# Optimization experiments

Measured on AMD Instinct MI355X. Metric: run time of the kernel, lower is better.

## Reference

```python
import jax, jax.numpy as jnp
import numpy as np

B, T, D, K = 64, 1024, 256, 1024
DECAY = 0.99      # ema_decay
BETA = 0.25       # commitment_cost
EPS = 1e-5


def setup_inputs() -> dict:
    key = jax.random.key(0)
    k1, k2 = jax.random.split(key, 2)
    z = jax.random.normal(k1, (B, T, D), dtype=jnp.float32)
    # nn.init.uniform_(embedding.weight, -1/K, 1/K)
    embed = jax.random.uniform(k2, (K, D), dtype=jnp.float32,
                               minval=-1.0 / K, maxval=1.0 / K)
    ema_count = jnp.zeros((K,), dtype=jnp.float32)
    ema_weight = embed  # buffer initialized as a clone of the weight
    return {"z": z, "embed": embed, "ema_count": ema_count, "ema_weight": ema_weight}


def reference(z, embed, ema_count, ema_weight):
    Bq, Tq, Dq = z.shape
    zf = z.reshape(-1, Dq)  # [N, D], N = B*T
    # squared euclidean distances: [N, K]
    dist = (zf * zf).sum(axis=1, keepdims=True) \
        - 2.0 * (zf @ embed.T) \
        + (embed * embed).sum(axis=1)
    idx = jnp.argmin(dist, axis=1)                      # [N]
    q = embed[idx].reshape(Bq, Tq, Dq)                  # nearest codebook vectors

    commit = jnp.mean((z - jax.lax.stop_gradient(q)) ** 2)
    codebook = jnp.mean((q - jax.lax.stop_gradient(z)) ** 2)
    vq_loss = codebook + BETA * commit

    # straight-through estimator
    q_st = z + jax.lax.stop_gradient(q - z)

    # EMA codebook update (training-mode, no_grad in torch)
    counts = jax.ops.segment_sum(jnp.ones((zf.shape[0],), zf.dtype), idx, num_segments=K)
    dw = jax.ops.segment_sum(zf, idx, num_segments=K)   # one_hot.T @ z_flat, [K, D]
    new_count = DECAY * ema_count + (1.0 - DECAY) * counts
    new_ema_w = DECAY * ema_weight + (1.0 - DECAY) * dw
    n = new_count.sum()
    cs = (new_count + EPS) / (n + K * EPS) * n          # laplace-smoothed counts
    new_embed = new_ema_w / cs[:, None]

    return (q_st, vq_loss, idx.reshape(Bq, Tq), new_embed, new_count, new_ema_w)
```

## Files before the change

### kernel.cpp

```cpp
#include <hip/hip_runtime.h>
#include <cfloat>

#define N_Q     65536
#define D_DIM   256
#define K_CODES 1024
#define DELTA   0.004f
#define MARGIN  0.001f
#define SW_CAP  1536
#define SPILL_CAP 65536

#define OUT_QST   0
#define OUT_LOSS  16777216
#define OUT_IDX   16777217
#define OUT_EMBED 16842753
#define OUT_COUNT 17104897
#define OUT_EMAW  17105921

#define WS_IDX    0u
#define WS_ZZ     262144u
#define WS_PERM   524288u
#define WS_PACK   786432u
#define WS_EN     1310720u
#define WS_ICNT   1314816u
#define WS_OFFS   1318912u
#define WS_OFFW   1323008u
#define WS_CNTF   1327104u
#define WS_CS     1331200u
#define WS_ET     1335296u
#define WS_LOSSB  1859584u
#define WS_SPCNT  1867776u

typedef short          bf16x8 __attribute__((ext_vector_type(8)));
typedef unsigned short u16x8  __attribute__((ext_vector_type(8)));
typedef float          f32x4  __attribute__((ext_vector_type(4)));

__device__ inline unsigned short f2bf(float x) {
    unsigned u = __float_as_uint(x);
    u += 0x7FFFu + ((u >> 16) & 1u);
    return (unsigned short)(u >> 16);
}
__device__ inline float bf2f(unsigned short h) {
    return __uint_as_float((unsigned)h << 16);
}
__device__ inline u16x8 pack8(float4 a, float4 b) {
    u16x8 p;
    p[0]=f2bf(a.x); p[1]=f2bf(a.y); p[2]=f2bf(a.z); p[3]=f2bf(a.w);
    p[4]=f2bf(b.x); p[5]=f2bf(b.y); p[6]=f2bf(b.z); p[7]=f2bf(b.w);
    return p;
}
__device__ inline void gll16(const void* g, void* l) {
    __builtin_amdgcn_global_load_lds(
        (const __attribute__((address_space(1))) unsigned int*)g,
        (__attribute__((address_space(3))) unsigned int*)l, 16, 0, 0);
}
#define DPPMIN(x, CTRL) fminf((x), __int_as_float( \
    __builtin_amdgcn_update_dpp(0, __float_as_int(x), (CTRL), 0xF, 0xF, false)))

__global__ void prep_kernel(const float* __restrict__ embed,
                            unsigned short* __restrict__ et,
                            unsigned long long* __restrict__ pack,
                            float* __restrict__ enorm,
                            int* __restrict__ icnt,
                            double* __restrict__ lossb,
                            int* __restrict__ spc)
{
    int b = blockIdx.x, t = threadIdx.x;
    if (b < 128) {
        int tid = b * 256 + t;
        int k16 = tid >> 9, d8 = (tid >> 4) & 31, col = tid & 15;
        const float* src = &embed[(size_t)(k16 * 16 + col) * D_DIM + d8 * 8];
        float4 a = *(const float4*)&src[0];
        float4 c = *(const float4*)&src[4];
        *(u16x8*)&et[(size_t)tid * 8] = pack8(a, c);
        unsigned long long* p = pack + (size_t)tid * 2;
        p[0] = ~0ull; p[1] = ~0ull;
    } else {
        int b2 = b - 128;
        int wave = t >> 6, lane = t & 63;
        int rbase = (b2 * 4 + wave) * 8;
        for (int i = 0; i < 8; ++i) {
            int r = rbase + i;
            const float4 v = *(const float4*)&embed[(size_t)r * D_DIM + lane * 4];
            float s = v.x * v.x + v.y * v.y + v.z * v.z + v.w * v.w;
            #pragma unroll
            for (int m = 32; m >= 1; m >>= 1) s += __shfl_down(s, m, 64);
            if (lane == 0) enorm[r] = s;
        }
        if (b2 == 0) {
            #pragma unroll
            for (int i = 0; i < 4; ++i) {
                icnt[t * 4 + i] = 0;
                lossb[t * 4 + i] = 0.0;
            }
            if (t == 0) *spc = 0;
        }
    }
}

__launch_bounds__(512, 4)
__global__ void sweep_kernel(const float* __restrict__ z,
                             const float* __restrict__ embed,
                             const unsigned short* __restrict__ et,
                             const float* __restrict__ enorm,
                             float* __restrict__ zzg,
                             unsigned long long* __restrict__ pack,
                             unsigned* __restrict__ spill,
                             int* __restrict__ spc)
{
    __shared__ unsigned short Eb[2][16384];
    __shared__ unsigned list[SW_CAP];
    __shared__ unsigned short s1h[SW_CAP];
    __shared__ float Ens[K_CODES];
    __shared__ float rminS[128];
    __shared__ float zzS[128];
    __shared__ int lcnt;

    const int t = threadIdx.x;
    const int w = t >> 6, lane = t & 63;
    const int col = lane & 15, quad = lane >> 4;
    const int qbase = blockIdx.x * 128;

    if (t == 0) lcnt = 0;
    for (int i = t; i < K_CODES; i += 512) Ens[i] = enorm[i];

    {
        const unsigned short* src = et + w * 2048 + lane * 8;
        unsigned short* dst = &Eb[0][w * 2048];
        #pragma unroll
        for (int i = 0; i < 4; ++i) gll16(src + i * 512, dst + i * 512);
    }

    bf16x8 A[8];
    {
        float s = 0.f;
        #pragma unroll
        for (int ds = 0; ds < 8; ++ds) {
            const float* zp = &z[(size_t)(qbase + w*16 + col) * D_DIM
                                 + ds*32 + quad*8];
            float4 a = *(const float4*)zp;
            float4 b = *(const float4*)(zp + 4);
            s += a.x*a.x + a.y*a.y + a.z*a.z + a.w*a.w
               + b.x*b.x + b.y*b.y + b.z*b.z + b.w*b.w;
            u16x8 p = pack8(a, b);
            A[ds] = *(bf16x8*)&p;
        }
        s += __shfl_xor(s, 16, 64);
        s += __shfl_xor(s, 32, 64);
        if (quad == 0) {
            zzg[qbase + w*16 + col] = s;
            zzS[w*16 + col] = s;
        }
    }

    float rmin[4];
    #pragma unroll
    for (int i = 0; i < 4; ++i) rmin[i] = FLT_MAX;

    asm volatile("s_waitcnt vmcnt(0) lgkmcnt(0)" ::: "memory");
    __builtin_amdgcn_s_barrier();
    __builtin_amdgcn_sched_barrier(0);

    #pragma unroll 1
    for (int kc = 0; kc < 16; ++kc) {
        if (kc < 15) {
            const unsigned short* src = et + (kc + 1) * 16384 + w * 2048 + lane * 8;
            unsigned short* dst = &Eb[(kc + 1) & 1][w * 2048];
            #pragma unroll
            for (int i = 0; i < 4; ++i) gll16(src + i * 512, dst + i * 512);
        }

        const unsigned short* buf = Eb[kc & 1];
        f32x4 acc[4];
        #pragma unroll
        for (int ct = 0; ct < 4; ++ct)
            acc[ct] = (f32x4){0.f, 0.f, 0.f, 0.f};

        #pragma unroll
        for (int ds = 0; ds < 8; ++ds) {
            bf16x8 B[4];
            #pragma unroll
            for (int ct = 0; ct < 4; ++ct)
                B[ct] = *(const bf16x8*)&buf[((ct*32 + ds*4 + quad)*16 + col)*8];
            #pragma unroll
            for (int ct = 0; ct < 4; ++ct)
                acc[ct] = __builtin_amdgcn_mfma_f32_16x16x32_bf16(A[ds], B[ct], acc[ct], 0, 0, 0);
        }

        float en4[4];
        #pragma unroll
        for (int ct = 0; ct < 4; ++ct) en4[ct] = Ens[kc*64 + ct*16 + col];

        float s1v[4][4];
        #pragma unroll
        for (int ct = 0; ct < 4; ++ct)
            #pragma unroll
            for (int rg = 0; rg < 4; ++rg)
                s1v[ct][rg] = fmaf(-2.0f, acc[ct][rg], en4[ct]);

        float m4[4];
        #pragma unroll
        for (int rg = 0; rg < 4; ++rg)
            m4[rg] = fminf(fminf(s1v[0][rg], s1v[1][rg]),
                           fminf(s1v[2][rg], s1v[3][rg]));

        #pragma unroll
        for (int i = 0; i < 4; ++i) m4[i] = DPPMIN(m4[i], 0xB1);
        #pragma unroll
        for (int i = 0; i < 4; ++i) m4[i] = DPPMIN(m4[i], 0x4E);
        #pragma unroll
        for (int i = 0; i < 4; ++i) m4[i] = DPPMIN(m4[i], 0x124);
        #pragma unroll
        for (int i = 0; i < 4; ++i) m4[i] = DPPMIN(m4[i], 0x128);

        float thrv[4];
        #pragma unroll
        for (int i = 0; i < 4; ++i) {
            rmin[i] = fminf(rmin[i], m4[i]);
            thrv[i] = rmin[i] + DELTA;
        }

        #pragma unroll
        for (int rg = 0; rg < 4; ++rg) {
            float th = thrv[rg];
            #pragma unroll
            for (int ct = 0; ct < 4; ++ct) {
                if (s1v[ct][rg] <= th) {
                    int k    = kc*64 + ct*16 + col;
                    int qloc = w*16 + quad*4 + rg;
                    int pos  = atomicAdd(&lcnt, 1);
                    if (pos < SW_CAP) {
                        list[pos] = ((unsigned)qloc << 10) | (unsigned)k;
                        s1h[pos]  = f2bf(s1v[ct][rg]);
                    } else {
                        int sp = atomicAdd(spc, 1);
                        if (sp < SPILL_CAP) {
                            spill[sp] = ((unsigned)(qbase + qloc) << 10)
                                      | (unsigned)k;
                            asm volatile("s_waitcnt vmcnt(0)" ::: "memory");
                        }
                    }
                }
            }
        }

        asm volatile("s_waitcnt vmcnt(4)" ::: "memory");
        __builtin_amdgcn_s_barrier();
        __builtin_amdgcn_sched_barrier(0);
    }

    if (col == 0) {
        #pragma unroll
        for (int rg = 0; rg < 4; ++rg)
            rminS[w*16 + quad*4 + rg] = rmin[rg];
    }
    asm volatile("s_waitcnt lgkmcnt(0)" ::: "memory");
    __builtin_amdgcn_s_barrier();
    __builtin_amdgcn_sched_barrier(0);
    asm volatile("" ::: "memory");

    int cnt = lcnt; if (cnt > SW_CAP) cnt = SW_CAP;
    int gid = t >> 3, gl = t & 7;
    for (int e = gid; e < cnt; e += 64) {
        unsigned ent = list[e];
        int qloc = (int)(ent >> 10), k = (int)(ent & 1023u);
        if (bf2f(s1h[e]) > rminS[qloc] + (DELTA + MARGIN)) continue;
        int qg = qbase + qloc;
        const float* zp  = &z[(size_t)qg * D_DIM + gl * 32];
        const float* epf = &embed[(size_t)k * D_DIM + gl * 32];
        double d0 = 0.0, d1 = 0.0;
        #pragma unroll
        for (int i = 0; i < 4; ++i) {
            float4 a  = *(const float4*)&zp[i*8];
            float4 b  = *(const float4*)&epf[i*8];
            float4 c  = *(const float4*)&zp[i*8 + 4];
            float4 dv = *(const float4*)&epf[i*8 + 4];
            d0 += (double)a.x*b.x + (double)a.y*b.y + (double)a.z*b.z + (double)a.w*b.w;
            d1 += (double)c.x*dv.x + (double)c.y*dv.y + (double)c.z*dv.z + (double)c.w*dv.w;
        }
        double dd = d0 + d1;
        #pragma unroll
        for (int m = 1; m < 8; m <<= 1) dd += __shfl_xor(dd, m, 64);
        if (gl == 0) {
            float s = (zzS[qloc] - 2.0f*(float)dd) + Ens[k];
            unsigned long long pk =
                ((unsigned long long)__float_as_uint(s) << 32) | (unsigned)k;
            atomicMin(&pack[qg], pk);
        }
    }
}

__global__ void spill_kernel(const float* __restrict__ z,
                             const float* __restrict__ embed,
                             const float* __restrict__ enorm,
                             const float* __restrict__ zz,
                             const unsigned* __restrict__ spill,
                             const int* __restrict__ spc,
                             unsigned long long* __restrict__ pack)
{
    int cnt = *spc; if (cnt > SPILL_CAP) cnt = SPILL_CAP;
    int gid = (blockIdx.x * 256 + threadIdx.x) >> 3, gl = threadIdx.x & 7;
    int stride = (gridDim.x * 256) >> 3;
    for (int e = gid; e < cnt; e += stride) {
        unsigned ent = spill[e];
        int qg = (int)(ent >> 10), k = (int)(ent & 1023u);
        const float* zp  = &z[(size_t)qg * D_DIM + gl * 32];
        const float* epf = &embed[(size_t)k * D_DIM + gl * 32];
        double dd = 0.0;
        #pragma unroll
        for (int i = 0; i < 8; ++i) {
            float4 a = *(const float4*)&zp[i*4];
            float4 b = *(const float4*)&epf[i*4];
            dd += (double)a.x*b.x + (double)a.y*b.y
                + (double)a.z*b.z + (double)a.w*b.w;
        }
        #pragma unroll
        for (int m = 1; m < 8; m <<= 1) dd += __shfl_xor(dd, m, 64);
        if (gl == 0) {
            float s = (zz[qg] - 2.0f*(float)dd) + enorm[k];
            unsigned long long pk =
                ((unsigned long long)__float_as_uint(s) << 32) | (unsigned)k;
            atomicMin(&pack[qg], pk);
        }
    }
}

__global__ void qst_unpack_kernel(const unsigned long long* __restrict__ pack,
                                  const float* __restrict__ z,
                                  const float* __restrict__ embed,
                                  int* __restrict__ idx_i,
                                  float* __restrict__ idx_f,
                                  int* __restrict__ icnt,
                                  float* __restrict__ qst,
                                  double* __restrict__ lossb)
{
    __shared__ int ks[4];
    int b = blockIdx.x, t = threadIdx.x;
    int n0 = b * 4;
    if (t < 4) {
        int k = (int)(pack[n0 + t] & 0xffffffffull);
        ks[t] = k;
        idx_i[n0 + t] = k;
        idx_f[n0 + t] = (float)k;
        atomicAdd(&icnt[k], 1);
    }
    __syncthreads();
    int e0 = b * 1024 + t * 4;
    int qi = t >> 6;
    int d  = (t * 4) & 255;
    int k  = ks[qi];
    const float4 q4 = *(const float4*)&embed[(size_t)k * D_DIM + d];
    const float4 z4 = *(const float4*)&z[e0];
    float4 o;
    o.x = z4.x + (q4.x - z4.x);
    o.y = z4.y + (q4.y - z4.y);
    o.z = z4.z + (q4.z - z4.z);
    o.w = z4.w + (q4.w - z4.w);
    *(float4*)&qst[e0] = o;
    float dx = z4.x - q4.x, dy = z4.y - q4.y, dz = z4.z - q4.z, dw = z4.w - q4.w;
    float s = dx * dx + dy * dy + dz * dz + dw * dw;
    #pragma unroll
    for (int m = 32; m >= 1; m >>= 1) s += __shfl_down(s, m, 64);
    __shared__ float ps[4];
    int wave = t >> 6, lane = t & 63;
    if (lane == 0) ps[wave] = s;
    __syncthreads();
    if (t == 0)
        atomicAdd(&lossb[b & 1023],
                  (double)((ps[0] + ps[1]) + (ps[2] + ps[3])));
}

__global__ void scan_kernel(const int* __restrict__ icnt,
                            int* __restrict__ offs,
                            int* __restrict__ offw,
                            float* __restrict__ cntf)
{
    __shared__ int s[1024];
    int t = threadIdx.x;
    int v0 = icnt[t];
    s[t] = v0;
    __syncthreads();
    for (int d = 1; d < 1024; d <<= 1) {
        int v = (t >= d) ? s[t - d] : 0;
        __syncthreads();
        s[t] += v;
        __syncthreads();
    }
    int excl = s[t] - v0;
    offs[t] = excl;
    offw[t] = excl;
    cntf[t] = (float)v0;
}

__global__ void fill_kernel(const int* __restrict__ idx,
                            int* __restrict__ offw,
                            int* __restrict__ perm)
{
    int n = blockIdx.x * 256 + threadIdx.x;
    int k = idx[n];
    int pos = atomicAdd(&offw[k], 1);
    perm[pos] = n;
}

__global__ void fin_counts_kernel(const float* __restrict__ ema_count,
                                  const float* __restrict__ cntf,
                                  const double* __restrict__ lossb,
                                  float* __restrict__ out_count,
                                  float* __restrict__ out_loss,
                                  float* __restrict__ cs)
{
    __shared__ float  red[1024];
    __shared__ double dred[1024];
    int t = threadIdx.x;
    float c = 0.99f * ema_count[t] + 0.01f * cntf[t];
    out_count[t] = c;
    red[t]  = c;
    dred[t] = lossb[t];
    __syncthreads();
    for (int s = 512; s >= 1; s >>= 1) {
        if (t < s) { red[t] += red[t + s]; dred[t] += dred[t + s]; }
        __syncthreads();
    }
    float n = red[0];
    cs[t] = (c + 1e-5f) / (n + 1024.0f * 1e-5f) * n;
    if (t == 0) {
        float m = (float)(dred[0] / (double)((size_t)N_Q * D_DIM));
        out_loss[0] = m + 0.25f * m;
    }
}

__global__ void accum_embed_kernel(const float* __restrict__ z,
                                   const int* __restrict__ perm,
                                   const int* __restrict__ icnt,
                                   const int* __restrict__ offs,
                                   const float* __restrict__ cs,
                                   const float* __restrict__ ema_w,
                                   float* __restrict__ out_embed,
                                   float* __restrict__ out_emaw)
{
    __shared__ int rows[256];
    int k = blockIdx.x, t = threadIdx.x;
    int cnt = icnt[k], off = offs[k];
    double a0 = 0.0, a1 = 0.0, a2 = 0.0, a3 = 0.0;
    for (int base = 0; base < cnt; base += 256) {
        int m = min(256, cnt - base);
        __syncthreads();
        if (t < m) rows[t] = perm[off + base + t];
        __syncthreads();
        int r = 0;
        for (; r + 4 <= m; r += 4) {
            a0 += (double)z[(size_t)rows[r+0] * D_DIM + t];
            a1 += (double)z[(size_t)rows[r+1] * D_DIM + t];
            a2 += (double)z[(size_t)rows[r+2] * D_DIM + t];
            a3 += (double)z[(size_t)rows[r+3] * D_DIM + t];
        }
        for (; r < m; ++r) a0 += (double)z[(size_t)rows[r] * D_DIM + t];
    }
    double acc = (a0 + a1) + (a2 + a3);
    float w = 0.99f * ema_w[(size_t)k * D_DIM + t] + 0.01f * (float)acc;
    out_emaw[(size_t)k * D_DIM + t]  = w;
    out_embed[(size_t)k * D_DIM + t] = w / cs[k];
}

extern "C" void kernel_launch(void* const* d_in, const int* in_sizes, int n_in,
                              void* d_out, int out_size, void* d_ws, size_t ws_size,
                              hipStream_t stream)
{
    const float* z          = (const float*)d_in[0];
    const float* embed      = (const float*)d_in[1];
    const float* ema_count  = (const float*)d_in[2];
    const float* ema_weight = (const float*)d_in[3];
    float* out = (float*)d_out;
    char*  ws  = (char*)d_ws;

    int*      ws_idx  = (int*)(ws + WS_IDX);
    unsigned* ws_spill= (unsigned*)(ws + WS_IDX);
    float*    ws_zz   = (float*)(ws + WS_ZZ);
    int*      ws_perm = (int*)(ws + WS_PERM);
    unsigned long long* ws_pack = (unsigned long long*)(ws + WS_PACK);
    float*    ws_en   = (float*)(ws + WS_EN);
    int*      ws_icnt = (int*)(ws + WS_ICNT);
    int*      ws_offs = (int*)(ws + WS_OFFS);
    int*      ws_offw = (int*)(ws + WS_OFFW);
    float*    ws_cntf = (float*)(ws + WS_CNTF);
    float*    ws_cs   = (float*)(ws + WS_CS);
    unsigned short* ws_et = (unsigned short*)(ws + WS_ET);
    double*   ws_lb   = (double*)(ws + WS_LOSSB);
    int*      ws_spc  = (int*)(ws + WS_SPCNT);

    prep_kernel<<<160, 256, 0, stream>>>(embed, ws_et, ws_pack, ws_en,
                                         ws_icnt, ws_lb, ws_spc);

    sweep_kernel<<<N_Q / 128, 512, 0, stream>>>(z, embed, ws_et, ws_en, ws_zz,
                                                ws_pack, ws_spill, ws_spc);

    spill_kernel<<<32, 256, 0, stream>>>(z, embed, ws_en, ws_zz,
                                         ws_spill, ws_spc, ws_pack);

    qst_unpack_kernel<<<N_Q / 4, 256, 0, stream>>>(ws_pack, z, embed,
                                                   ws_idx, out + OUT_IDX,
                                                   ws_icnt, out + OUT_QST, ws_lb);
    scan_kernel<<<1, 1024, 0, stream>>>(ws_icnt, ws_offs, ws_offw, ws_cntf);
    fill_kernel<<<N_Q / 256, 256, 0, stream>>>(ws_idx, ws_offw, ws_perm);
    fin_counts_kernel<<<1, 1024, 0, stream>>>(ema_count, ws_cntf, ws_lb,
                                              out + OUT_COUNT, out + OUT_LOSS, ws_cs);
    accum_embed_kernel<<<K_CODES, 256, 0, stream>>>(z, ws_perm, ws_icnt, ws_offs,
                                                    ws_cs, ema_weight,
                                                    out + OUT_EMBED, out + OUT_EMAW);
}
```

Measured before the change: 271.4 us.

## Switch sweep to 32x32 MFMA tiles and split codebook across two block sets

The sweep kernel now uses 32x32x16 bf16 MFMA with 256 queries per block. The codebook is split into two halves of 512 codes, each handled by a separate set of blocks, so the grid stays at 512 blocks. The prep kernel re-lays out the bf16 codebook to match the new B-operand fragment order, and the candidate list capacity is doubled. This is meant to cut LDS traffic per FLOP and raise MFMA efficiency. In exchange each query's z tile is loaded and converted twice, each set finds only a partial row minimum so more candidates pass the threshold, the per-stage wait becomes a full vmcnt(0), and register pressure rises with 16 A fragments and 16 running minima.

```diff
diff --git a/kernel.cpp b/kernel.cpp
--- a/kernel.cpp
+++ b/kernel.cpp
@@ -6,7 +6,7 @@
 #define K_CODES 1024
 #define DELTA   0.004f
 #define MARGIN  0.001f
-#define SW_CAP  1536
+#define SW_CAP  3072
 #define SPILL_CAP 65536
 
 #define OUT_QST   0
@@ -32,7 +32,7 @@
 
 typedef short          bf16x8 __attribute__((ext_vector_type(8)));
 typedef unsigned short u16x8  __attribute__((ext_vector_type(8)));
-typedef float          f32x4  __attribute__((ext_vector_type(4)));
+typedef float          f32x16 __attribute__((ext_vector_type(16)));
 
 __device__ inline unsigned short f2bf(float x) {
     unsigned u = __float_as_uint(x);
@@ -67,8 +67,11 @@
     int b = blockIdx.x, t = threadIdx.x;
     if (b < 128) {
         int tid = b * 256 + t;
-        int k16 = tid >> 9, d8 = (tid >> 4) & 31, col = tid & 15;
-        const float* src = &embed[(size_t)(k16 * 16 + col) * D_DIM + d8 * 8];
+        int g = tid >> 10, rem = tid & 1023;
+        int s = rem >> 6, lane = rem & 63;
+        int row = g * 32 + (lane & 31);
+        int d0  = s * 16 + (lane >> 5) * 8;
+        const float* src = &embed[(size_t)row * D_DIM + d0];
         float4 a = *(const float4*)&src[0];
         float4 c = *(const float4*)&src[4];
         *(u16x8*)&et[(size_t)tid * 8] = pack8(a, c);
@@ -107,54 +110,55 @@
                              unsigned* __restrict__ spill,
                              int* __restrict__ spc)
 {
-    __shared__ unsigned short Eb[2][16384];
+    __shared__ unsigned short Eb[2][8192];
     __shared__ unsigned list[SW_CAP];
     __shared__ unsigned short s1h[SW_CAP];
-    __shared__ float Ens[K_CODES];
-    __shared__ float rminS[128];
-    __shared__ float zzS[128];
+    __shared__ float Ens[512];
+    __shared__ float rminS[256];
+    __shared__ float zzS[256];
     __shared__ int lcnt;
 
     const int t = threadIdx.x;
     const int w = t >> 6, lane = t & 63;
-    const int col = lane & 15, quad = lane >> 4;
-    const int qbase = blockIdx.x * 128;
+    const int c32 = lane & 31, hi = lane >> 5;
+    const int set = blockIdx.x >> 8;
+    const int qb  = blockIdx.x & 255;
+    const int qbase = qb * 256;
+    const int koff  = set * 512;
 
     if (t == 0) lcnt = 0;
-    for (int i = t; i < K_CODES; i += 512) Ens[i] = enorm[i];
+    Ens[t] = enorm[koff + t];
 
     {
-        const unsigned short* src = et + w * 2048 + lane * 8;
-        unsigned short* dst = &Eb[0][w * 2048];
-        #pragma unroll
-        for (int i = 0; i < 4; ++i) gll16(src + i * 512, dst + i * 512);
-    }
-
-    bf16x8 A[8];
+        const unsigned short* src = et + (size_t)(set*16 + 0) * 8192 + w*1024 + lane*8;
+        unsigned short* dst = &Eb[0][w * 1024];
+        gll16(src, dst);
+        gll16(src + 512, dst + 512);
+    }
+
+    bf16x8 Aq[16];
     {
-        float s = 0.f;
-        #pragma unroll
-        for (int ds = 0; ds < 8; ++ds) {
-            const float* zp = &z[(size_t)(qbase + w*16 + col) * D_DIM
-                                 + ds*32 + quad*8];
-            float4 a = *(const float4*)zp;
-            float4 b = *(const float4*)(zp + 4);
-            s += a.x*a.x + a.y*a.y + a.z*a.z + a.w*a.w
-               + b.x*b.x + b.y*b.y + b.z*b.z + b.w*b.w;
+        const float* zrow = &z[(size_t)(qbase + w*32 + c32) * D_DIM + hi*8];
+        float s2 = 0.f;
+        #pragma unroll
+        for (int s = 0; s < 16; ++s) {
+            float4 a = *(const float4*)&zrow[s*16];
+            float4 b = *(const float4*)&zrow[s*16 + 4];
+            s2 += a.x*a.x + a.y*a.y + a.z*a.z + a.w*a.w
+                + b.x*b.x + b.y*b.y + b.z*b.z + b.w*b.w;
             u16x8 p = pack8(a, b);
-            A[ds] = *(bf16x8*)&p;
-        }
-        s += __shfl_xor(s, 16, 64);
-        s += __shfl_xor(s, 32, 64);
-        if (quad == 0) {
-            zzg[qbase + w*16 + col] = s;
-            zzS[w*16 + col] = s;
-        }
-    }
-
-    float rmin[4];
+            Aq[s] = *(bf16x8*)&p;
+        }
+        float zz = s2 + __shfl_xor(s2, 32, 64);
+        if (lane < 32) {
+            zzS[w*32 + c32] = zz;
+            if (set == 0) zzg[qbase + w*32 + c32] = zz;
+        }
+    }
+
+    float rmin[16];
     #pragma unroll
-    for (int i = 0; i < 4; ++i) rmin[i] = FLT_MAX;
+    for (int r = 0; r < 16; ++r) rmin[r] = FLT_MAX;
 
     asm volatile("s_waitcnt vmcnt(0) lgkmcnt(0)" ::: "memory");
     __builtin_amdgcn_s_barrier();
@@ -163,100 +167,70 @@
     #pragma unroll 1
     for (int kc = 0; kc < 16; ++kc) {
         if (kc < 15) {
-            const unsigned short* src = et + (kc + 1) * 16384 + w * 2048 + lane * 8;
-            unsigned short* dst = &Eb[(kc + 1) & 1][w * 2048];
-            #pragma unroll
-            for (int i = 0; i < 4; ++i) gll16(src + i * 512, dst + i * 512);
+            const unsigned short* src =
+                et + (size_t)(set*16 + kc + 1) * 8192 + w*1024 + lane*8;
+            unsigned short* dst = &Eb[(kc + 1) & 1][w * 1024];
+            gll16(src, dst);
+            gll16(src + 512, dst + 512);
         }
 
         const unsigned short* buf = Eb[kc & 1];
-        f32x4 acc[4];
-        #pragma unroll
-        for (int ct = 0; ct < 4; ++ct)
-            acc[ct] = (f32x4){0.f, 0.f, 0.f, 0.f};
-
-        #pragma unroll
-        for (int ds = 0; ds < 8; ++ds) {
-            bf16x8 B[4];
-            #pragma unroll
-            for (int ct = 0; ct < 4; ++ct)
-                B[ct] = *(const bf16x8*)&buf[((ct*32 + ds*4 + quad)*16 + col)*8];
-            #pragma unroll
-            for (int ct = 0; ct < 4; ++ct)
-                acc[ct] = __builtin_amdgcn_mfma_f32_16x16x32_bf16(A[ds], B[ct], acc[ct], 0, 0, 0);
-        }
-
-        float en4[4];
-        #pragma unroll
-        for (int ct = 0; ct < 4; ++ct) en4[ct] = Ens[kc*64 + ct*16 + col];
-
-        float s1v[4][4];
-        #pragma unroll
-        for (int ct = 0; ct < 4; ++ct)
-            #pragma unroll
-            for (int rg = 0; rg < 4; ++rg)
-                s1v[ct][rg] = fmaf(-2.0f, acc[ct][rg], en4[ct]);
-
-        float m4[4];
-        #pragma unroll
-        for (int rg = 0; rg < 4; ++rg)
-            m4[rg] = fminf(fminf(s1v[0][rg], s1v[1][rg]),
-                           fminf(s1v[2][rg], s1v[3][rg]));
-
-        #pragma unroll
-        for (int i = 0; i < 4; ++i) m4[i] = DPPMIN(m4[i], 0xB1);
-        #pragma unroll
-        for (int i = 0; i < 4; ++i) m4[i] = DPPMIN(m4[i], 0x4E);
-        #pragma unroll
-        for (int i = 0; i < 4; ++i) m4[i] = DPPMIN(m4[i], 0x124);
-        #pragma unroll
-        for (int i = 0; i < 4; ++i) m4[i] = DPPMIN(m4[i], 0x128);
-
-        float thrv[4];
-        #pragma unroll
-        for (int i = 0; i < 4; ++i) {
-            rmin[i] = fminf(rmin[i], m4[i]);
-            thrv[i] = rmin[i] + DELTA;
-        }
-
-        #pragma unroll
-        for (int rg = 0; rg < 4; ++rg) {
-            float th = thrv[rg];
-            #pragma unroll
-            for (int ct = 0; ct < 4; ++ct) {
-                if (s1v[ct][rg] <= th) {
-                    int k    = kc*64 + ct*16 + col;
-                    int qloc = w*16 + quad*4 + rg;
-                    int pos  = atomicAdd(&lcnt, 1);
-                    if (pos < SW_CAP) {
-                        list[pos] = ((unsigned)qloc << 10) | (unsigned)k;
-                        s1h[pos]  = f2bf(s1v[ct][rg]);
-                    } else {
-                        int sp = atomicAdd(spc, 1);
-                        if (sp < SPILL_CAP) {
-                            spill[sp] = ((unsigned)(qbase + qloc) << 10)
-                                      | (unsigned)k;
-                            asm volatile("s_waitcnt vmcnt(0)" ::: "memory");
-                        }
+        f32x16 acc;
+        #pragma unroll
+        for (int i = 0; i < 16; ++i) acc[i] = 0.f;
+
+        #pragma unroll
+        for (int s = 0; s < 16; ++s) {
+            bf16x8 B = *(const bf16x8*)&buf[s*512 + lane*8];
+            acc = __builtin_amdgcn_mfma_f32_32x32x16_bf16(Aq[s], B, acc, 0, 0, 0);
+        }
+
+        float en = Ens[kc*32 + c32];
+        acc = en - 2.0f * acc;
+
+        #pragma unroll
+        for (int r = 0; r < 16; ++r) {
+            float mv = acc[r];
+            mv = DPPMIN(mv, 0xB1);
+            mv = DPPMIN(mv, 0x4E);
+            mv = DPPMIN(mv, 0x124);
+            mv = DPPMIN(mv, 0x128);
+            rmin[r] = fminf(rmin[r], mv);
+            float th = rmin[r] + DELTA;
+            if (acc[r] <= th) {
+                int k    = koff + kc*32 + c32;
+                int qloc = w*32 + (r & 3) + 8*(r >> 2) + 4*hi;
+                int pos  = atomicAdd(&lcnt, 1);
+                if (pos < SW_CAP) {
+                    list[pos] = ((unsigned)qloc << 10) | (unsigned)k;
+                    s1h[pos]  = f2bf(acc[r]);
+                } else {
+                    int sp = atomicAdd(spc, 1);
+                    if (sp < SPILL_CAP) {
+                        spill[sp] = ((unsigned)(qbase + qloc) << 10)
+                                  | (unsigned)k;
+                        asm volatile("s_waitcnt vmcnt(0)" ::: "memory");
                     }
                 }
             }
         }
 
-        asm volatile("s_waitcnt vmcnt(4)" ::: "memory");
+        asm volatile("s_waitcnt vmcnt(0)" ::: "memory");
         __builtin_amdgcn_s_barrier();
         __builtin_amdgcn_sched_barrier(0);
     }
 
-    if (col == 0) {
-        #pragma unroll
-        for (int rg = 0; rg < 4; ++rg)
-            rminS[w*16 + quad*4 + rg] = rmin[rg];
+    #pragma unroll
+    for (int r = 0; r < 16; ++r)
+        rmin[r] = fminf(rmin[r], __shfl_xor(rmin[r], 16, 64));
+    if (c32 == 0) {
+        #pragma unroll
+        for (int r = 0; r < 16; ++r)
+            rminS[w*32 + (r & 3) + 8*(r >> 2) + 4*hi] = rmin[r];
     }
     asm volatile("s_waitcnt lgkmcnt(0)" ::: "memory");
     __builtin_amdgcn_s_barrier();
     __builtin_amdgcn_sched_barrier(0);
-    asm volatile("" ::: "memory");
 
     int cnt = lcnt; if (cnt > SW_CAP) cnt = SW_CAP;
     int gid = t >> 3, gl = t & 7;
@@ -281,7 +255,7 @@
         #pragma unroll
         for (int m = 1; m < 8; m <<= 1) dd += __shfl_xor(dd, m, 64);
         if (gl == 0) {
-            float s = (zzS[qloc] - 2.0f*(float)dd) + Ens[k];
+            float s = (zzS[qloc] - 2.0f*(float)dd) + Ens[k & 511];
             unsigned long long pk =
                 ((unsigned long long)__float_as_uint(s) << 32) | (unsigned)k;
             atomicMin(&pack[qg], pk);
@@ -490,8 +464,8 @@
     prep_kernel<<<160, 256, 0, stream>>>(embed, ws_et, ws_pack, ws_en,
                                          ws_icnt, ws_lb, ws_spc);
 
-    sweep_kernel<<<N_Q / 128, 512, 0, stream>>>(z, embed, ws_et, ws_en, ws_zz,
-                                                ws_pack, ws_spill, ws_spc);
+    sweep_kernel<<<512, 512, 0, stream>>>(z, embed, ws_et, ws_en, ws_zz,
+                                          ws_pack, ws_spill, ws_spc);
 
     spill_kernel<<<32, 256, 0, stream>>>(z, embed, ws_en, ws_zz,
                                          ws_spill, ws_spc, ws_pack);
```

Result: slower. 378.1 us (+39.3%).

## Halve sweep codebook chunk for higher occupancy and fuse scan with count finalization

Applied to the files above, without the earlier changes.

The sweep kernel now streams the bf16 codebook in 32-code chunks instead of 64, halving the double-buffered LDS tile and the accumulator registers, and raises the launch-bounds occupancy hint from 4 to 6 blocks. This aims to fit more blocks per CU to hide latency, at the cost of twice as many loop iterations, barriers and DPP min reductions. Separately, the single-block scan and count-finalization kernels are merged into one launch, dropping a kernel launch and the intermediate float count buffer.

```diff
diff --git a/kernel.cpp b/kernel.cpp
--- a/kernel.cpp
+++ b/kernel.cpp
@@ -97,7 +97,7 @@
     }
 }
 
-__launch_bounds__(512, 4)
+__launch_bounds__(512, 6)
 __global__ void sweep_kernel(const float* __restrict__ z,
                              const float* __restrict__ embed,
                              const unsigned short* __restrict__ et,
@@ -107,7 +107,7 @@
                              unsigned* __restrict__ spill,
                              int* __restrict__ spc)
 {
-    __shared__ unsigned short Eb[2][16384];
+    __shared__ unsigned short Eb[2][8192];
     __shared__ unsigned list[SW_CAP];
     __shared__ unsigned short s1h[SW_CAP];
     __shared__ float Ens[K_CODES];
@@ -124,10 +124,10 @@
     for (int i = t; i < K_CODES; i += 512) Ens[i] = enorm[i];
 
     {
-        const unsigned short* src = et + w * 2048 + lane * 8;
-        unsigned short* dst = &Eb[0][w * 2048];
-        #pragma unroll
-        for (int i = 0; i < 4; ++i) gll16(src + i * 512, dst + i * 512);
+        const unsigned short* src = et + w * 1024 + lane * 8;
+        unsigned short* dst = &Eb[0][w * 1024];
+        gll16(src, dst);
+        gll16(src + 512, dst + 512);
     }
 
     bf16x8 A[8];
@@ -161,47 +161,43 @@
     __builtin_amdgcn_sched_barrier(0);
 
     #pragma unroll 1
-    for (int kc = 0; kc < 16; ++kc) {
-        if (kc < 15) {
-            const unsigned short* src = et + (kc + 1) * 16384 + w * 2048 + lane * 8;
-            unsigned short* dst = &Eb[(kc + 1) & 1][w * 2048];
-            #pragma unroll
-            for (int i = 0; i < 4; ++i) gll16(src + i * 512, dst + i * 512);
+    for (int kc = 0; kc < 32; ++kc) {
+        if (kc < 31) {
+            const unsigned short* src = et + (kc + 1) * 8192 + w * 1024 + lane * 8;
+            unsigned short* dst = &Eb[(kc + 1) & 1][w * 1024];
+            gll16(src, dst);
+            gll16(src + 512, dst + 512);
         }
 
         const unsigned short* buf = Eb[kc & 1];
-        f32x4 acc[4];
-        #pragma unroll
-        for (int ct = 0; ct < 4; ++ct)
+        f32x4 acc[2];
+        #pragma unroll
+        for (int ct = 0; ct < 2; ++ct)
             acc[ct] = (f32x4){0.f, 0.f, 0.f, 0.f};
 
         #pragma unroll
         for (int ds = 0; ds < 8; ++ds) {
-            bf16x8 B[4];
-            #pragma unroll
-            for (int ct = 0; ct < 4; ++ct)
-                B[ct] = *(const bf16x8*)&buf[((ct*32 + ds*4 + quad)*16 + col)*8];
-            #pragma unroll
-            for (int ct = 0; ct < 4; ++ct)
-                acc[ct] = __builtin_amdgcn_mfma_f32_16x16x32_bf16(A[ds], B[ct], acc[ct], 0, 0, 0);
-        }
-
-        float en4[4];
-        #pragma unroll
-        for (int ct = 0; ct < 4; ++ct) en4[ct] = Ens[kc*64 + ct*16 + col];
-
-        float s1v[4][4];
-        #pragma unroll
-        for (int ct = 0; ct < 4; ++ct)
+            bf16x8 B0 = *(const bf16x8*)&buf[((      ds*4 + quad)*16 + col)*8];
+            bf16x8 B1 = *(const bf16x8*)&buf[((32 + ds*4 + quad)*16 + col)*8];
+            acc[0] = __builtin_amdgcn_mfma_f32_16x16x32_bf16(A[ds], B0, acc[0], 0, 0, 0);
+            acc[1] = __builtin_amdgcn_mfma_f32_16x16x32_bf16(A[ds], B1, acc[1], 0, 0, 0);
+        }
+
+        float en2[2];
+        #pragma unroll
+        for (int ct = 0; ct < 2; ++ct) en2[ct] = Ens[kc*32 + ct*16 + col];
+
+        float s1v[2][4];
+        #pragma unroll
+        for (int ct = 0; ct < 2; ++ct)
             #pragma unroll
             for (int rg = 0; rg < 4; ++rg)
-                s1v[ct][rg] = fmaf(-2.0f, acc[ct][rg], en4[ct]);
+                s1v[ct][rg] = fmaf(-2.0f, acc[ct][rg], en2[ct]);
 
         float m4[4];
         #pragma unroll
         for (int rg = 0; rg < 4; ++rg)
-            m4[rg] = fminf(fminf(s1v[0][rg], s1v[1][rg]),
-                           fminf(s1v[2][rg], s1v[3][rg]));
+            m4[rg] = fminf(s1v[0][rg], s1v[1][rg]);
 
         #pragma unroll
         for (int i = 0; i < 4; ++i) m4[i] = DPPMIN(m4[i], 0xB1);
@@ -223,9 +219,9 @@
         for (int rg = 0; rg < 4; ++rg) {
             float th = thrv[rg];
             #pragma unroll
-            for (int ct = 0; ct < 4; ++ct) {
+            for (int ct = 0; ct < 2; ++ct) {
                 if (s1v[ct][rg] <= th) {
-                    int k    = kc*64 + ct*16 + col;
+                    int k    = kc*32 + ct*16 + col;
                     int qloc = w*16 + quad*4 + rg;
                     int pos  = atomicAdd(&lcnt, 1);
                     if (pos < SW_CAP) {
@@ -243,7 +239,7 @@
             }
         }
 
-        asm volatile("s_waitcnt vmcnt(4)" ::: "memory");
+        asm volatile("s_waitcnt vmcnt(2)" ::: "memory");
         __builtin_amdgcn_s_barrier();
         __builtin_amdgcn_sched_barrier(0);
     }
@@ -369,12 +365,18 @@
                   (double)((ps[0] + ps[1]) + (ps[2] + ps[3])));
 }
 
-__global__ void scan_kernel(const int* __restrict__ icnt,
-                            int* __restrict__ offs,
-                            int* __restrict__ offw,
-                            float* __restrict__ cntf)
+__global__ void scan_fin_kernel(const int* __restrict__ icnt,
+                                const float* __restrict__ ema_count,
+                                const double* __restrict__ lossb,
+                                int* __restrict__ offs,
+                                int* __restrict__ offw,
+                                float* __restrict__ out_count,
+                                float* __restrict__ out_loss,
+                                float* __restrict__ cs)
 {
     __shared__ int s[1024];
+    __shared__ float  red[1024];
+    __shared__ double dred[1024];
     int t = threadIdx.x;
     int v0 = icnt[t];
     s[t] = v0;
@@ -388,36 +390,13 @@
     int excl = s[t] - v0;
     offs[t] = excl;
     offw[t] = excl;
-    cntf[t] = (float)v0;
-}
-
-__global__ void fill_kernel(const int* __restrict__ idx,
-                            int* __restrict__ offw,
-                            int* __restrict__ perm)
-{
-    int n = blockIdx.x * 256 + threadIdx.x;
-    int k = idx[n];
-    int pos = atomicAdd(&offw[k], 1);
-    perm[pos] = n;
-}
-
-__global__ void fin_counts_kernel(const float* __restrict__ ema_count,
-                                  const float* __restrict__ cntf,
-                                  const double* __restrict__ lossb,
-                                  float* __restrict__ out_count,
-                                  float* __restrict__ out_loss,
-                                  float* __restrict__ cs)
-{
-    __shared__ float  red[1024];
-    __shared__ double dred[1024];
-    int t = threadIdx.x;
-    float c = 0.99f * ema_count[t] + 0.01f * cntf[t];
+    float c = 0.99f * ema_count[t] + 0.01f * (float)v0;
     out_count[t] = c;
     red[t]  = c;
     dred[t] = lossb[t];
     __syncthreads();
-    for (int s = 512; s >= 1; s >>= 1) {
-        if (t < s) { red[t] += red[t + s]; dred[t] += dred[t + s]; }
+    for (int sh = 512; sh >= 1; sh >>= 1) {
+        if (t < sh) { red[t] += red[t + sh]; dred[t] += dred[t + sh]; }
         __syncthreads();
     }
     float n = red[0];
@@ -426,6 +405,16 @@
         float m = (float)(dred[0] / (double)((size_t)N_Q * D_DIM));
         out_loss[0] = m + 0.25f * m;
     }
+}
+
+__global__ void fill_kernel(const int* __restrict__ idx,
+                            int* __restrict__ offw,
+                            int* __restrict__ perm)
+{
+    int n = blockIdx.x * 256 + threadIdx.x;
+    int k = idx[n];
+    int pos = atomicAdd(&offw[k], 1);
+    perm[pos] = n;
 }
 
 __global__ void accum_embed_kernel(const float* __restrict__ z,
@@ -481,7 +470,6 @@
     int*      ws_icnt = (int*)(ws + WS_ICNT);
     int*      ws_offs = (int*)(ws + WS_OFFS);
     int*      ws_offw = (int*)(ws + WS_OFFW);
-    float*    ws_cntf = (float*)(ws + WS_CNTF);
     float*    ws_cs   = (float*)(ws + WS_CS);
     unsigned short* ws_et = (unsigned short*)(ws + WS_ET);
     double*   ws_lb   = (double*)(ws + WS_LOSSB);
@@ -499,10 +487,10 @@
     qst_unpack_kernel<<<N_Q / 4, 256, 0, stream>>>(ws_pack, z, embed,
                                                    ws_idx, out + OUT_IDX,
                                                    ws_icnt, out + OUT_QST, ws_lb);
-    scan_kernel<<<1, 1024, 0, stream>>>(ws_icnt, ws_offs, ws_offw, ws_cntf);
+    scan_fin_kernel<<<1, 1024, 0, stream>>>(ws_icnt, ema_count, ws_lb,
+                                            ws_offs, ws_offw,
+                                            out + OUT_COUNT, out + OUT_LOSS, ws_cs);
     fill_kernel<<<N_Q / 256, 256, 0, stream>>>(ws_idx, ws_offw, ws_perm);
-    fin_counts_kernel<<<1, 1024, 0, stream>>>(ema_count, ws_cntf, ws_lb,
-                                              out + OUT_COUNT, out + OUT_LOSS, ws_cs);
     accum_embed_kernel<<<K_CODES, 256, 0, stream>>>(z, ws_perm, ws_icnt, ws_offs,
                                                     ws_cs, ema_weight,
                                                     out + OUT_EMBED, out + OUT_EMAW);
```

Measured after the change: 297.4 us. +9.6%, slower.
